# Optimization experiments

Measured on AMD Instinct MI355X. Metric: run time of the kernel, lower is better.

Reference implementation:

```python
import jax, jax.numpy as jnp
import numpy as np

N = 200          # fixed by map_norm's .view(200, 1)
D = 8192         # in_features
EPS = 1e-5


def setup_inputs() -> dict:
    key = jax.random.key(0)
    ks = jax.random.split(key, 7)
    lim = float(np.sqrt(6.0 / D))
    x = jax.random.normal(ks[0], (N, D), dtype=jnp.float32)
    Wq = jax.random.uniform(ks[1], (D, D), dtype=jnp.float32, minval=-lim, maxval=lim)
    Wk = jax.random.uniform(ks[2], (D, D), dtype=jnp.float32, minval=-lim, maxval=lim)
    Wv = jax.random.uniform(ks[3], (D, D), dtype=jnp.float32, minval=-lim, maxval=lim)
    bq = jax.random.normal(ks[4], (D,), dtype=jnp.float32) * 0.01
    bk = jax.random.normal(ks[5], (D,), dtype=jnp.float32) * 0.01
    bv = jax.random.normal(ks[6], (D,), dtype=jnp.float32) * 0.01
    return {"x": x, "Wq": Wq, "bq": bq, "Wk": Wk, "bk": bk, "Wv": Wv, "bv": bv}


def reference(x, Wq, bq, Wk, bk, Wv, bv):
    d_out = x.shape[1]
    cc = jnp.sqrt(jnp.asarray(d_out, dtype=x.dtype))
    # nn.Linear: y = x @ W.T + b
    q = x @ Wq.T + bq          # [N, D]
    k = x @ Wk.T + bk          # [N, D]
    v = x @ Wv.T + bv          # [N, D]
    s = q @ k.T                # [N, N] score map
    mean = jnp.mean(s, axis=-1, keepdims=True)
    var = jnp.var(s, axis=-1, keepdims=True, ddof=1)  # torch.var is unbiased
    s = (s - mean) / jnp.sqrt(var + EPS)
    s = jnp.sin(s)
    scores = jax.nn.softmax(s / cc, axis=-1)
    return scores @ v          # [N, D]
```

## Files before the change

### kernel.cpp

```cpp
#include <hip/hip_runtime.h>
#include <hip/hip_bf16.h>
#include <cstdint>

#define DD 8192
#define NROW 200
#define MT 13
#define MPAD 208
#define KPV 256
#define EPSV 1e-5f
#define BK 64
#define MT7 7
#define ABUF_BYTES (MPAD * BK * 2)

using short8 = __attribute__((ext_vector_type(8))) short;
using f32x4  = __attribute__((ext_vector_type(4))) float;

__device__ __forceinline__ ushort f2bf(float f) {
    union { float f; unsigned u; } c; c.f = f;
    unsigned u = c.u;
    return (ushort)((u + 0x7FFFu + ((u >> 16) & 1u)) >> 16);
}

__device__ __forceinline__ short8 pack8(float4 a, float4 b) {
    short8 o;
    o[0]=f2bf(a.x); o[1]=f2bf(a.y); o[2]=f2bf(a.z); o[3]=f2bf(a.w);
    o[4]=f2bf(b.x); o[5]=f2bf(b.y); o[6]=f2bf(b.z); o[7]=f2bf(b.w);
    return o;
}

__device__ __forceinline__ short8 pack8f(f32x4 a, f32x4 b) {
    short8 o;
    union { __hip_bfloat162 h; unsigned u; } q;
    q.h = __float22bfloat162_rn(float2{a[0], a[1]}); o[0]=(short)(q.u & 0xffff); o[1]=(short)(q.u >> 16);
    q.h = __float22bfloat162_rn(float2{a[2], a[3]}); o[2]=(short)(q.u & 0xffff); o[3]=(short)(q.u >> 16);
    q.h = __float22bfloat162_rn(float2{b[0], b[1]}); o[4]=(short)(q.u & 0xffff); o[5]=(short)(q.u >> 16);
    q.h = __float22bfloat162_rn(float2{b[2], b[3]}); o[6]=(short)(q.u & 0xffff); o[7]=(short)(q.u >> 16);
    return o;
}

__global__ void cvt_x(const float* __restrict__ x, ushort* __restrict__ xb) {
    int i = (blockIdx.x * 256 + threadIdx.x) * 8;
    int row = i >> 13;
    int col = i & (DD - 1);
    short8 o;
    if (row < NROW) {
        const float4* p = reinterpret_cast<const float4*>(x + (size_t)row * DD + col);
        float4 a = p[0], b = p[1];
        o = pack8(a, b);
    } else {
        for (int j = 0; j < 8; ++j) o[j] = 0;
    }
    *reinterpret_cast<short8*>(xb + i) = o;
}

#define GL(dst, ptr, OFF) \
    asm volatile("global_load_dwordx4 %0, %1, off offset:" #OFF \
                 : "=&v"(dst) : "v"(ptr) : "memory")
#define WAITV(N) asm volatile("s_waitcnt vmcnt(" #N ")" ::: "memory")
#define SB __builtin_amdgcn_sched_barrier(0)
#define RAWBAR asm volatile("s_barrier" ::: "memory")

__global__ __launch_bounds__(768) void qkv_w12(
    const ushort* __restrict__ xb,
    const float* __restrict__ Wq, const float* __restrict__ Wk, const float* __restrict__ Wv,
    const float* __restrict__ bq, const float* __restrict__ bk, const float* __restrict__ bv,
    ushort* __restrict__ qb, ushort* __restrict__ kb, ushort* __restrict__ vt)
{
    __shared__ char L[2 * ABUF_BYTES];

    const int cb   = blockIdx.x;
    const int t    = threadIdx.x;
    const int lane = t & 63;
    const int wave = t >> 6;
    const int mat  = wave >> 2;
    const int cg   = (wave >> 1) & 1;
    const int mh   = wave & 1;
    const int c    = lane & 15;
    const int kgrp = lane >> 4;
    const int ncol = cb * 32 + cg * 16 + c;

    const float* W    = (mat == 0) ? Wq : (mat == 1 ? Wk : Wv);
    const float* bias = (mat == 0) ? bq : (mat == 1 ? bk : bv);
    const float* wq   = W + (size_t)ncol * DD + kgrp * 8;

    const ushort* sbase = xb + (size_t)(lane >> 3) * DD
                             + (size_t)(((lane & 7) ^ ((lane >> 3) & 7)) * 8);

    const int b0off = c * 128 + ((kgrp ^ (c & 7)) * 16);
    const int b1off = b0off ^ 64;

    f32x4 acc[MT7];
    #pragma unroll
    for (int m = 0; m < MT7; ++m)
        for (int r = 0; r < 4; ++r) acc[m][r] = 0.f;

    f32x4 uA0, uA1, uA2, uA3, uB0, uB1, uB2, uB3;

#define STAGE(B, KK) { if (wave < 6) { _Pragma("unroll") for (int j = 0; j < 5; ++j) { \
        int g = wave + 6 * j; \
        if (g < 26) { \
            __builtin_amdgcn_global_load_lds( \
                (const __attribute__((address_space(1))) void*)(sbase + (KK) + (size_t)g * 8 * DD), \
                (__attribute__((address_space(3))) void*)(L + (B) + g * 1024), \
                16, 0, 0); } } } }

#define COMPUTE(RB, bb0, bb1) { _Pragma("unroll") for (int m = 0; m < MT7; ++m) { \
        int tt = mh * 6 + m; \
        short8 a0 = *reinterpret_cast<const short8*>(L + (RB) + tt * 2048 + b0off); \
        acc[m] = __builtin_amdgcn_mfma_f32_16x16x32_bf16(a0, bb0, acc[m], 0, 0, 0); \
        short8 a1 = *reinterpret_cast<const short8*>(L + (RB) + tt * 2048 + b1off); \
        acc[m] = __builtin_amdgcn_mfma_f32_16x16x32_bf16(a1, bb1, acc[m], 0, 0, 0); } }

#define PHASE(RB, UC) { \
        STAGE((RB) ^ ABUF_BYTES, kn); \
        kn = (kn + BK) & (DD - 1); \
        if (wave >= 6)     { WAITV(4); } \
        else if (wave < 2) { WAITV(9); } \
        else               { WAITV(8); } \
        SB; \
        short8 bb0 = pack8f(UC##0, UC##1); \
        short8 bb1 = pack8f(UC##2, UC##3); \
        GL(UC##0, wq + k2, 0); \
        GL(UC##1, wq + k2, 16); \
        GL(UC##2, wq + k2, 128); \
        GL(UC##3, wq + k2, 144); \
        k2 = (k2 + BK) & (DD - 1); \
        RAWBAR; \
        COMPUTE(RB, bb0, bb1); \
        asm volatile("s_waitcnt lgkmcnt(0)" ::: "memory"); \
        RAWBAR; }

    int kn = BK;
    int k2 = 2 * BK;
    STAGE(0, 0);
    GL(uA0, wq, 0);  GL(uA1, wq, 16);  GL(uA2, wq, 128);  GL(uA3, wq, 144);
    GL(uB0, wq + BK, 0); GL(uB1, wq + BK, 16); GL(uB2, wq + BK, 128); GL(uB3, wq + BK, 144);

    #pragma unroll 1
    for (int it = 0; it < DD / (2 * BK); ++it) {
        PHASE(0, uA);
        PHASE(ABUF_BYTES, uB);
    }
#undef PHASE
#undef COMPUTE
#undef STAGE

    asm volatile("s_waitcnt vmcnt(0) lgkmcnt(0)" ::: "memory");
    RAWBAR;

    const float bv0 = bias[ncol];
    if (mat < 2) {
        ushort* outb = (mat == 0) ? qb : kb;
        #pragma unroll
        for (int m = 0; m < MT7; ++m) {
            if (m >= mh) {
                #pragma unroll
                for (int r = 0; r < 4; ++r) {
                    int row = (mh * 6 + m) * 16 + kgrp * 4 + r;
                    outb[(size_t)row * DD + ncol] = f2bf(acc[m][r] + bv0);
                }
            }
        }
    } else {
        #pragma unroll
        for (int m = 0; m < MT7; ++m) {
            if (m >= mh) {
                #pragma unroll
                for (int r = 0; r < 4; ++r) {
                    int row = (mh * 6 + m) * 16 + kgrp * 4 + r;
                    vt[(size_t)ncol * KPV + row] = f2bf(acc[m][r] + bv0);
                }
            }
        }
    }
}

__global__ __launch_bounds__(256) void sgemm(const ushort* __restrict__ qb, const ushort* __restrict__ kb,
                                             float* __restrict__ sbuf) {
    const int bm = blockIdx.y, bn = blockIdx.x;
    const int lane  = threadIdx.x & 63;
    const int wave  = threadIdx.x >> 6;
    const int col16 = lane & 15, kgrp = lane >> 4;
    const ushort* ap = qb + (size_t)(bm * 16 + col16) * DD + kgrp * 8;
    const ushort* bp = kb + (size_t)(bn * 16 + col16) * DD + kgrp * 8;
    f32x4 acc;
    for (int r = 0; r < 4; ++r) acc[r] = 0.f;
    const int kend = (wave + 1) * 2048;
    for (int k0 = wave * 2048; k0 < kend; k0 += 32) {
        short8 a = *reinterpret_cast<const short8*>(ap + k0);
        short8 b = *reinterpret_cast<const short8*>(bp + k0);
        acc = __builtin_amdgcn_mfma_f32_16x16x32_bf16(a, b, acc, 0, 0, 0);
    }
    __shared__ f32x4 red[4][64];
    red[wave][lane] = acc;
    __syncthreads();
    if (wave == 0) {
        f32x4 s = red[0][lane];
        for (int j = 1; j < 4; ++j) { f32x4 o = red[j][lane]; for (int r = 0; r < 4; ++r) s[r] += o[r]; }
        for (int r = 0; r < 4; ++r)
            sbuf[(size_t)(bm * 16 + kgrp * 4 + r) * MPAD + bn * 16 + col16] = s[r];
    }
}

__global__ __launch_bounds__(256) void rownorm(const float* __restrict__ sbuf, ushort* __restrict__ pb) {
    const int row = blockIdx.x;
    const int t = threadIdx.x;
    if (row >= NROW) { pb[(size_t)row * KPV + t] = 0; return; }
    __shared__ float part[4];
    const int lane = t & 63, wave = t >> 6;
    float x = (t < NROW) ? sbuf[(size_t)row * MPAD + t] : 0.f;

    float s = x;
    for (int m = 32; m; m >>= 1) s += __shfl_xor(s, m, 64);
    if (lane == 0) part[wave] = s;
    __syncthreads();
    float mean = (part[0] + part[1] + part[2] + part[3]) * (1.f / 200.f);

    float d = (t < NROW) ? (x - mean) : 0.f;
    float s2 = d * d;
    for (int m = 32; m; m >>= 1) s2 += __shfl_xor(s2, m, 64);
    __syncthreads();
    if (lane == 0) part[wave] = s2;
    __syncthreads();
    float var = (part[0] + part[1] + part[2] + part[3]) * (1.f / 199.f);

    float inv = 1.f / sqrtf(var + EPSV);
    float y = sinf(d * inv);
    const float inv_cc = 1.f / 90.50966799187809f;
    float e = (t < NROW) ? expf(y * inv_cc) : 0.f;

    float se = e;
    for (int m = 32; m; m >>= 1) se += __shfl_xor(se, m, 64);
    __syncthreads();
    if (lane == 0) part[wave] = se;
    __syncthreads();
    float tot = part[0] + part[1] + part[2] + part[3];
    pb[(size_t)row * KPV + t] = (t < NROW) ? f2bf(e / tot) : (ushort)0;
}

__global__ __launch_bounds__(256) void pv_gemm(const ushort* __restrict__ pb, const ushort* __restrict__ vt,
                                               float* __restrict__ out) {
    const int lane  = threadIdx.x & 63;
    const int wave  = threadIdx.x >> 6;
    const int col16 = lane & 15, kgrp = lane >> 4;
    const int ncol  = blockIdx.x * 64 + wave * 16 + col16;
    const ushort* ap = pb + (size_t)col16 * KPV + kgrp * 8;
    const ushort* bp = vt + (size_t)ncol  * KPV + kgrp * 8;
    f32x4 acc[MT];
    for (int m = 0; m < MT; ++m)
        for (int r = 0; r < 4; ++r) acc[m][r] = 0.f;
    for (int k0 = 0; k0 < KPV; k0 += 32) {
        short8 b = *reinterpret_cast<const short8*>(bp + k0);
        #pragma unroll
        for (int m = 0; m < MT; ++m) {
            short8 a = *reinterpret_cast<const short8*>(ap + (size_t)m * 16 * KPV + k0);
            acc[m] = __builtin_amdgcn_mfma_f32_16x16x32_bf16(a, b, acc[m], 0, 0, 0);
        }
    }
    for (int m = 0; m < MT; ++m)
        for (int r = 0; r < 4; ++r) {
            int row = m * 16 + kgrp * 4 + r;
            if (row < NROW) out[(size_t)row * DD + ncol] = acc[m][r];
        }
}

extern "C" void kernel_launch(void* const* d_in, const int* in_sizes, int n_in,
                              void* d_out, int out_size, void* d_ws, size_t ws_size,
                              hipStream_t stream) {
    const float* x  = (const float*)d_in[0];
    const float* Wq = (const float*)d_in[1];
    const float* bq = (const float*)d_in[2];
    const float* Wk = (const float*)d_in[3];
    const float* bk = (const float*)d_in[4];
    const float* Wv = (const float*)d_in[5];
    const float* bv = (const float*)d_in[6];
    float* out = (float*)d_out;

    char* ws = (char*)d_ws;
    ushort* xb   = (ushort*)(ws);
    ushort* qb   = (ushort*)(ws + 3407872);
    ushort* kb   = (ushort*)(ws + 6815744);
    ushort* vt   = (ushort*)(ws + 10223616);
    float*  sbuf = (float*)(ws + 14417920);
    ushort* pb   = (ushort*)(ws + 14590976);

    cvt_x<<<832, 256, 0, stream>>>(x, xb);
    qkv_w12<<<256, 768, 0, stream>>>(xb, Wq, Wk, Wv, bq, bk, bv, qb, kb, vt);
    sgemm<<<dim3(13, 13), 256, 0, stream>>>(qb, kb, sbuf);
    rownorm<<<208, 256, 0, stream>>>(sbuf, pb);
    pv_gemm<<<128, 256, 0, stream>>>(pb, vt, out);
}
```

Baseline: 288.1 us.

## Halve waves in QKV kernel, each wave computes two 16-column tiles

The fused QKV projection kernel drops from 12 to 6 waves per block. Each wave now computes two 16-column output tiles, reusing every LDS-loaded A fragment for two MFMAs and issuing twice as many weight loads per phase. All 6 waves share the x-tile staging, and the vmcnt waits are retuned to match. This cuts LDS reads per FLOP and barrier participants, but doubles accumulator and prefetch register use per wave and reduces the wave count available to hide weight-streaming latency.

```diff
diff --git a/kernel.cpp b/kernel.cpp
--- a/kernel.cpp
+++ b/kernel.cpp
@@ -60,7 +60,7 @@
 #define SB __builtin_amdgcn_sched_barrier(0)
 #define RAWBAR asm volatile("s_barrier" ::: "memory")
 
-__global__ __launch_bounds__(768) void qkv_w12(
+__global__ __launch_bounds__(384) void qkv_h2(
     const ushort* __restrict__ xb,
     const float* __restrict__ Wq, const float* __restrict__ Wk, const float* __restrict__ Wv,
     const float* __restrict__ bq, const float* __restrict__ bk, const float* __restrict__ bv,
@@ -72,16 +72,17 @@
     const int t    = threadIdx.x;
     const int lane = t & 63;
     const int wave = t >> 6;
-    const int mat  = wave >> 2;
-    const int cg   = (wave >> 1) & 1;
+    const int mat  = wave >> 1;
     const int mh   = wave & 1;
     const int c    = lane & 15;
     const int kgrp = lane >> 4;
-    const int ncol = cb * 32 + cg * 16 + c;
+    const int ncol0 = cb * 32 + c;
+    const int ncol1 = ncol0 + 16;
 
     const float* W    = (mat == 0) ? Wq : (mat == 1 ? Wk : Wv);
     const float* bias = (mat == 0) ? bq : (mat == 1 ? bk : bv);
-    const float* wq   = W + (size_t)ncol * DD + kgrp * 8;
+    const float* wp0  = W + (size_t)ncol0 * DD + kgrp * 8;
+    const float* wp1  = W + (size_t)ncol1 * DD + kgrp * 8;
 
     const ushort* sbase = xb + (size_t)(lane >> 3) * DD
                              + (size_t)(((lane & 7) ^ ((lane >> 3) & 7)) * 8);
@@ -89,52 +90,61 @@
     const int b0off = c * 128 + ((kgrp ^ (c & 7)) * 16);
     const int b1off = b0off ^ 64;
 
-    f32x4 acc[MT7];
+    f32x4 acc0[MT7], acc1[MT7];
     #pragma unroll
     for (int m = 0; m < MT7; ++m)
-        for (int r = 0; r < 4; ++r) acc[m][r] = 0.f;
-
-    f32x4 uA0, uA1, uA2, uA3, uB0, uB1, uB2, uB3;
-
-#define STAGE(B, KK) { if (wave < 6) { _Pragma("unroll") for (int j = 0; j < 5; ++j) { \
+        for (int r = 0; r < 4; ++r) { acc0[m][r] = 0.f; acc1[m][r] = 0.f; }
+
+    f32x4 uA0, uA1, uA2, uA3, uA4, uA5, uA6, uA7;
+    f32x4 uB0, uB1, uB2, uB3, uB4, uB5, uB6, uB7;
+
+#define STAGE(B, KK) { _Pragma("unroll") for (int j = 0; j < 5; ++j) { \
         int g = wave + 6 * j; \
         if (g < 26) { \
             __builtin_amdgcn_global_load_lds( \
                 (const __attribute__((address_space(1))) void*)(sbase + (KK) + (size_t)g * 8 * DD), \
                 (__attribute__((address_space(3))) void*)(L + (B) + g * 1024), \
-                16, 0, 0); } } } }
-
-#define COMPUTE(RB, bb0, bb1) { _Pragma("unroll") for (int m = 0; m < MT7; ++m) { \
+                16, 0, 0); } } }
+
+#define COMPUTE(RB, b00, b01, b10, b11) { _Pragma("unroll") for (int m = 0; m < MT7; ++m) { \
         int tt = mh * 6 + m; \
         short8 a0 = *reinterpret_cast<const short8*>(L + (RB) + tt * 2048 + b0off); \
-        acc[m] = __builtin_amdgcn_mfma_f32_16x16x32_bf16(a0, bb0, acc[m], 0, 0, 0); \
+        acc0[m] = __builtin_amdgcn_mfma_f32_16x16x32_bf16(a0, b00, acc0[m], 0, 0, 0); \
+        acc1[m] = __builtin_amdgcn_mfma_f32_16x16x32_bf16(a0, b10, acc1[m], 0, 0, 0); \
         short8 a1 = *reinterpret_cast<const short8*>(L + (RB) + tt * 2048 + b1off); \
-        acc[m] = __builtin_amdgcn_mfma_f32_16x16x32_bf16(a1, bb1, acc[m], 0, 0, 0); } }
+        acc0[m] = __builtin_amdgcn_mfma_f32_16x16x32_bf16(a1, b01, acc0[m], 0, 0, 0); \
+        acc1[m] = __builtin_amdgcn_mfma_f32_16x16x32_bf16(a1, b11, acc1[m], 0, 0, 0); } }
 
 #define PHASE(RB, UC) { \
         STAGE((RB) ^ ABUF_BYTES, kn); \
         kn = (kn + BK) & (DD - 1); \
-        if (wave >= 6)     { WAITV(4); } \
-        else if (wave < 2) { WAITV(9); } \
-        else               { WAITV(8); } \
+        if (wave < 2) { WAITV(13); } else { WAITV(12); } \
         SB; \
-        short8 bb0 = pack8f(UC##0, UC##1); \
-        short8 bb1 = pack8f(UC##2, UC##3); \
-        GL(UC##0, wq + k2, 0); \
-        GL(UC##1, wq + k2, 16); \
-        GL(UC##2, wq + k2, 128); \
-        GL(UC##3, wq + k2, 144); \
+        short8 b00 = pack8f(UC##0, UC##1); \
+        short8 b01 = pack8f(UC##2, UC##3); \
+        short8 b10 = pack8f(UC##4, UC##5); \
+        short8 b11 = pack8f(UC##6, UC##7); \
+        GL(UC##0, wp0 + k2, 0); \
+        GL(UC##1, wp0 + k2, 16); \
+        GL(UC##2, wp0 + k2, 128); \
+        GL(UC##3, wp0 + k2, 144); \
+        GL(UC##4, wp1 + k2, 0); \
+        GL(UC##5, wp1 + k2, 16); \
+        GL(UC##6, wp1 + k2, 128); \
+        GL(UC##7, wp1 + k2, 144); \
         k2 = (k2 + BK) & (DD - 1); \
         RAWBAR; \
-        COMPUTE(RB, bb0, bb1); \
+        COMPUTE(RB, b00, b01, b10, b11); \
         asm volatile("s_waitcnt lgkmcnt(0)" ::: "memory"); \
         RAWBAR; }
 
     int kn = BK;
     int k2 = 2 * BK;
     STAGE(0, 0);
-    GL(uA0, wq, 0);  GL(uA1, wq, 16);  GL(uA2, wq, 128);  GL(uA3, wq, 144);
-    GL(uB0, wq + BK, 0); GL(uB1, wq + BK, 16); GL(uB2, wq + BK, 128); GL(uB3, wq + BK, 144);
+    GL(uA0, wp0, 0);  GL(uA1, wp0, 16);  GL(uA2, wp0, 128);  GL(uA3, wp0, 144);
+    GL(uA4, wp1, 0);  GL(uA5, wp1, 16);  GL(uA6, wp1, 128);  GL(uA7, wp1, 144);
+    GL(uB0, wp0 + BK, 0);  GL(uB1, wp0 + BK, 16);  GL(uB2, wp0 + BK, 128);  GL(uB3, wp0 + BK, 144);
+    GL(uB4, wp1 + BK, 0);  GL(uB5, wp1 + BK, 16);  GL(uB6, wp1 + BK, 128);  GL(uB7, wp1 + BK, 144);
 
     #pragma unroll 1
     for (int it = 0; it < DD / (2 * BK); ++it) {
@@ -148,7 +158,8 @@
     asm volatile("s_waitcnt vmcnt(0) lgkmcnt(0)" ::: "memory");
     RAWBAR;
 
-    const float bv0 = bias[ncol];
+    const float bv0 = bias[ncol0];
+    const float bv1 = bias[ncol1];
     if (mat < 2) {
         ushort* outb = (mat == 0) ? qb : kb;
         #pragma unroll
@@ -157,7 +168,8 @@
                 #pragma unroll
                 for (int r = 0; r < 4; ++r) {
                     int row = (mh * 6 + m) * 16 + kgrp * 4 + r;
-                    outb[(size_t)row * DD + ncol] = f2bf(acc[m][r] + bv0);
+                    outb[(size_t)row * DD + ncol0] = f2bf(acc0[m][r] + bv0);
+                    outb[(size_t)row * DD + ncol1] = f2bf(acc1[m][r] + bv1);
                 }
             }
         }
@@ -168,7 +180,8 @@
                 #pragma unroll
                 for (int r = 0; r < 4; ++r) {
                     int row = (mh * 6 + m) * 16 + kgrp * 4 + r;
-                    vt[(size_t)ncol * KPV + row] = f2bf(acc[m][r] + bv0);
+                    vt[(size_t)ncol0 * KPV + row] = f2bf(acc0[m][r] + bv0);
+                    vt[(size_t)ncol1 * KPV + row] = f2bf(acc1[m][r] + bv1);
                 }
             }
         }
@@ -285,7 +298,7 @@
     ushort* pb   = (ushort*)(ws + 14590976);
 
     cvt_x<<<832, 256, 0, stream>>>(x, xb);
-    qkv_w12<<<256, 768, 0, stream>>>(xb, Wq, Wk, Wv, bq, bk, bv, qb, kb, vt);
+    qkv_h2<<<256, 384, 0, stream>>>(xb, Wq, Wk, Wv, bq, bk, bv, qb, kb, vt);
     sgemm<<<dim3(13, 13), 256, 0, stream>>>(qb, kb, sbuf);
     rownorm<<<208, 256, 0, stream>>>(sbuf, pb);
     pv_gemm<<<128, 256, 0, stream>>>(pb, vt, out);
```

Result: no change. 289.1 us (+0.3%).
